# Performance work log

Hardware: AMD Instinct MI355X
Metric: run time of the kernel (lower is better)

## Reference

```python
import jax, jax.numpy as jnp
import numpy as np

N = 60000    # total nodes
E = 600000   # total edges
R = 7        # num relations (edge types)
D_IN = 64    # raw node feature dim
D = 128      # hidden_channels
D2 = 64      # hidden_channels // 2
L = 2        # num_layers
EPS = 1e-5   # LayerNorm eps (torch default)


def setup_inputs() -> dict:
    key = jax.random.key(0)
    ks = jax.random.split(key, 10)
    s = 0.05  # xavier-ish scale
    return {
        "x": jax.random.normal(ks[0], (N, D_IN), jnp.float32),
        "edge_index": jax.random.randint(ks[1], (2, E), 0, N, dtype=jnp.int64),
        "edge_type": jax.random.randint(ks[2], (E,), 0, R, dtype=jnp.int64),
        "emb_W": jax.random.normal(ks[3], (D_IN, D), jnp.float32) * s,
        "emb_b": jnp.zeros((D,), jnp.float32),
        "rel_W": jax.random.normal(ks[4], (L, R, D, D), jnp.float32) * s,
        "root_W": jax.random.normal(ks[5], (L, D, D), jnp.float32) * s,
        "conv_b": jnp.zeros((L, D), jnp.float32),
        "ln_g": jnp.ones((L, D), jnp.float32),
        "ln_b": jnp.zeros((L, D), jnp.float32),
        "cls_W1": jax.random.normal(ks[6], (D, D2), jnp.float32) * s,
        "cls_b1": jnp.zeros((D2,), jnp.float32),
        "cls_ln_g": jnp.ones((D2,), jnp.float32),
        "cls_ln_b": jnp.zeros((D2,), jnp.float32),
        "cls_W2": jax.random.normal(ks[7], (D2, 1), jnp.float32) * s,
        "cls_b2": jnp.zeros((1,), jnp.float32),
    }


def _layernorm(h, g, b):
    m = h.mean(-1, keepdims=True)
    v = h.var(-1, keepdims=True)  # population variance, matches torch LayerNorm
    return (h - m) * jax.lax.rsqrt(v + EPS) * g + b


def _rgcn_conv(h, Wrel, Wroot, b, src, dst, edge_type):
    # Transform every node by every relation weight: [R*N, D]
    t = jnp.einsum('nd,rde->rne', h, Wrel).reshape(R * N, D)
    msg = t[edge_type * N + src]                      # [E, D] per-edge messages
    seg = edge_type * N + dst                         # per-(relation, dst) segments
    summed = jax.ops.segment_sum(msg, seg, num_segments=R * N)
    cnt = jax.ops.segment_sum(jnp.ones((E,), msg.dtype), seg, num_segments=R * N)
    mean = summed / jnp.maximum(cnt, 1.0)[:, None]    # scatter-mean per relation
    agg = mean.reshape(R, N, D).sum(0)                # sum over relations
    return agg + h @ Wroot + b


def reference(x, edge_index, edge_type, emb_W, emb_b, rel_W, root_W, conv_b,
              ln_g, ln_b, cls_W1, cls_b1, cls_ln_g, cls_ln_b, cls_W2, cls_b2):
    src, dst = edge_index[0], edge_index[1]
    # Node embedding (features clamped as in original forward)
    h = jnp.clip(x, -10.0, 10.0) @ emb_W + emb_b
    for l in range(L):
        h = _rgcn_conv(h, rel_W[l], root_W[l], conv_b[l], src, dst, edge_type)
        h = jax.nn.relu(_layernorm(h, ln_g[l], ln_b[l]))
        # dropout is identity at inference
    # Classifier on transaction nodes (= all nodes in this unified setup)
    z = jax.nn.relu(_layernorm(h @ cls_W1 + cls_b1, cls_ln_g, cls_ln_b))
    return z @ cls_W2 + cls_b2  # [N, 1] logits
```

## Files before the change

### kernel.cpp

```cpp
#include <hip/hip_runtime.h>
#include <hip/hip_bf16.h>

typedef unsigned int uint;
typedef unsigned short ushort;

#define N_NODES 60000
#define N_EDGES 600000
#define NREL 7
#define D_IN 64
#define DHID 128
#define LEPS 1e-5f
#define EMB_BLKS 938
#define ROW_BLKS 469
#define SCAT_BLKS 512

typedef __attribute__((ext_vector_type(8))) short bf16x8v;
typedef __attribute__((ext_vector_type(4))) float f32x4v;

#define AS1C(p) ((const __attribute__((address_space(1))) void*)(p))
#define AS3(p)  ((__attribute__((address_space(3))) void*)(p))

__device__ __forceinline__ float bf2f(uint u16) {
    return __uint_as_float(u16 << 16);
}
__device__ __forceinline__ uint f2bf(float f) {
    uint u = __float_as_uint(f);
    uint lsb = (u >> 16) & 1u;
    u += 0x7fffu + lsb;
    return u >> 16;
}
__device__ __forceinline__ uint pack2(float a, float b) {
    return f2bf(a) | (f2bf(b) << 16);
}

__global__ __launch_bounds__(256) void k_prep(const float* __restrict__ relW,
                                              const float* __restrict__ rootW,
                                              const float* __restrict__ embW,
                                              const int* __restrict__ dst,
                                              const int* __restrict__ et,
                                              ushort* __restrict__ Btr,
                                              ushort* __restrict__ Bte,
                                              int* __restrict__ deg8) {
    __shared__ float t[64][65];
    const int tid = threadIdx.x;
    if (blockIdx.x < 64) {
        const int l  = blockIdx.x >> 5;
        const int b5 = blockIdx.x & 31;
        const int r  = b5 >> 2;
        const int kt = (b5 >> 1) & 1;
        const int jt = b5 & 1;
        #pragma unroll
        for (int i = 0; i < 4; ++i) {
            const int idx = i * 256 + tid;
            const int kr = idx >> 4;
            const int j4 = idx & 15;
            const int kg = kt * 64 + kr;
            const float* src = (r < 7)
                ? (relW + (((size_t)l * 7 + r) * 128 + kg) * 128 + jt * 64 + j4 * 4)
                : (rootW + ((size_t)l * 128 + kg) * 128 + jt * 64 + j4 * 4);
            const float4 v = *(const float4*)src;
            t[kr][j4 * 4 + 0] = v.x; t[kr][j4 * 4 + 1] = v.y;
            t[kr][j4 * 4 + 2] = v.z; t[kr][j4 * 4 + 3] = v.w;
        }
        __syncthreads();
        uint* btd = (uint*)Btr;
        #pragma unroll
        for (int i = 0; i < 8; ++i) {
            const int idx = i * 256 + tid;
            const int jr = idx >> 5;
            const int kd = idx & 31;
            const uint w = pack2(t[kd * 2][jr], t[kd * 2 + 1][jr]);
            btd[((size_t)(l * 8 + r) * 128 + jt * 64 + jr) * 64 + kt * 32 + kd] = w;
        }
    } else if (blockIdx.x < 66) {
        const int jt = blockIdx.x - 64;
        #pragma unroll
        for (int i = 0; i < 4; ++i) {
            const int idx = i * 256 + tid;
            const int kr = idx >> 4;
            const int j4 = idx & 15;
            const float4 v = *(const float4*)(embW + (size_t)kr * 128 + jt * 64 + j4 * 4);
            t[kr][j4 * 4 + 0] = v.x; t[kr][j4 * 4 + 1] = v.y;
            t[kr][j4 * 4 + 2] = v.z; t[kr][j4 * 4 + 3] = v.w;
        }
        __syncthreads();
        uint* btd = (uint*)Bte;
        #pragma unroll
        for (int i = 0; i < 8; ++i) {
            const int idx = i * 256 + tid;
            const int jr = idx >> 5;
            const int kd = idx & 31;
            const uint w = pack2(t[kd * 2][jr], t[kd * 2 + 1][jr]);
            btd[(size_t)(jt * 64 + jr) * 32 + kd] = w;
        }
    } else {
        for (int e = (blockIdx.x - 66) * 256 + tid; e < N_EDGES; e += 1024 * 256)
            atomicAdd(&deg8[dst[e] * 8 + et[e]], 1);
    }
}

__global__ void k_scan1n(const int* __restrict__ deg8, int* __restrict__ rp,
                         int* __restrict__ bsum, int n) {
    __shared__ int s[256];
    const int t = threadIdx.x;
    const int i = blockIdx.x * 256 + t;
    int v = 0;
    if (i < n) {
        const int4 x = *(const int4*)(deg8 + (size_t)i * 8);
        const int4 y = *(const int4*)(deg8 + (size_t)i * 8 + 4);
        v = x.x + x.y + x.z + x.w + y.x + y.y + y.z + y.w;
    }
    s[t] = v;
    __syncthreads();
    for (int o = 1; o < 256; o <<= 1) {
        int uu = (t >= o) ? s[t - o] : 0;
        __syncthreads();
        s[t] += uu;
        __syncthreads();
    }
    if (i < n) rp[i] = s[t] - v;
    if (t == 255) bsum[blockIdx.x] = s[255];
}
__global__ void k_scanmid(int* __restrict__ bs, int nb) {
    __shared__ int s[256];
    __shared__ int carrys;
    const int t = threadIdx.x;
    if (t == 0) carrys = 0;
    __syncthreads();
    const int nch = (nb + 255) / 256;
    for (int ch = 0; ch < nch; ++ch) {
        const int i = ch * 256 + t;
        const int v = (i < nb) ? bs[i] : 0;
        s[t] = v;
        __syncthreads();
        for (int o = 1; o < 256; o <<= 1) {
            int uu = (t >= o) ? s[t - o] : 0;
            __syncthreads();
            s[t] += uu;
            __syncthreads();
        }
        const int carry = carrys;
        if (i < nb) bs[i] = s[t] - v + carry;
        __syncthreads();
        if (t == 255) carrys = carry + s[255];
        __syncthreads();
    }
}
__global__ void k_scanadd(int* __restrict__ a, const int* __restrict__ bsums,
                          int* __restrict__ fill, int n) {
    const int i = blockIdx.x * 256 + threadIdx.x;
    if (i < n) {
        const int v = a[i] + bsums[blockIdx.x];
        a[i] = v;
        fill[i] = v;
    }
    if (blockIdx.x == 0 && threadIdx.x == 0) a[n] = N_EDGES;
}

__global__ __launch_bounds__(256) void k_emb(const float* __restrict__ x,
                                             const ushort* __restrict__ Bte,
                                             const float* __restrict__ ebias,
                                             ushort* __restrict__ h) {
    __shared__ alignas(16) ushort sa[64 * 64];
    __shared__ alignas(16) ushort sb[128 * 64];
    const int tid = threadIdx.x;
    const int lane = tid & 63;
    const int wid = tid >> 6;
    const int wrow = wid >> 1, wcol = wid & 1;
    const int l15 = lane & 15, lh = lane >> 4;
    const int row0 = blockIdx.x * 64;

    #pragma unroll
    for (int i = 0; i < 2; ++i) {
        const int p = i * 256 + tid;
        const int row = p >> 3, gq = p & 7;
        const int n = min(row0 + row, N_NODES - 1);
        const float4 xa = *(const float4*)(x + (size_t)n * 64 + gq * 8);
        const float4 xb = *(const float4*)(x + (size_t)n * 64 + gq * 8 + 4);
        uint w[4];
        w[0] = pack2(fminf(fmaxf(xa.x, -10.f), 10.f), fminf(fmaxf(xa.y, -10.f), 10.f));
        w[1] = pack2(fminf(fmaxf(xa.z, -10.f), 10.f), fminf(fmaxf(xa.w, -10.f), 10.f));
        w[2] = pack2(fminf(fmaxf(xb.x, -10.f), 10.f), fminf(fmaxf(xb.y, -10.f), 10.f));
        w[3] = pack2(fminf(fmaxf(xb.z, -10.f), 10.f), fminf(fmaxf(xb.w, -10.f), 10.f));
        *(uint4*)&sa[(row * 8 + (gq ^ (row & 7))) * 8] = make_uint4(w[0], w[1], w[2], w[3]);
    }
    #pragma unroll
    for (int i = 0; i < 4; ++i) {
        const int p = i * 256 + tid;
        const int row = p >> 3, gq = p & 7;
        const uint4 v = *(const uint4*)((const uint*)Bte + (size_t)row * 32 + gq * 4);
        *(uint4*)&sb[(row * 8 + (gq ^ (row & 7))) * 8] = v;
    }
    float bv[4];
    #pragma unroll
    for (int fn = 0; fn < 4; ++fn) bv[fn] = ebias[wcol * 64 + fn * 16 + l15];
    __syncthreads();

    f32x4v acc[2][4];
    #pragma unroll
    for (int fm = 0; fm < 2; ++fm)
        #pragma unroll
        for (int fn = 0; fn < 4; ++fn)
            acc[fm][fn] = (f32x4v){0.f, 0.f, 0.f, 0.f};
    #pragma unroll
    for (int kh = 0; kh < 2; ++kh) {
        bf16x8v af[2], bfr[4];
        #pragma unroll
        for (int fm = 0; fm < 2; ++fm) {
            const int rowa = wrow * 32 + fm * 16 + l15;
            const int slot = (kh * 4 + lh) ^ (rowa & 7);
            af[fm] = *(const bf16x8v*)&sa[rowa * 64 + slot * 8];
        }
        #pragma unroll
        for (int fn = 0; fn < 4; ++fn) {
            const int rowb = wcol * 64 + fn * 16 + l15;
            const int slot = (kh * 4 + lh) ^ (rowb & 7);
            bfr[fn] = *(const bf16x8v*)&sb[rowb * 64 + slot * 8];
        }
        #pragma unroll
        for (int fm = 0; fm < 2; ++fm)
            #pragma unroll
            for (int fn = 0; fn < 4; ++fn)
                acc[fm][fn] = __builtin_amdgcn_mfma_f32_16x16x32_bf16(
                    af[fm], bfr[fn], acc[fm][fn], 0, 0, 0);
    }
    #pragma unroll
    for (int fm = 0; fm < 2; ++fm)
        #pragma unroll
        for (int r = 0; r < 4; ++r) {
            const int row = row0 + wrow * 32 + fm * 16 + lh * 4 + r;
            if (row < N_NODES) {
                #pragma unroll
                for (int fn = 0; fn < 4; ++fn) {
                    const int col = wcol * 64 + fn * 16 + l15;
                    h[(size_t)row * 128 + col] = (ushort)f2bf(acc[fm][fn][r] + bv[fn]);
                }
            }
        }
}

__global__ __launch_bounds__(512) void k_transcat(const ushort* __restrict__ h16,
                                                  const ushort* __restrict__ Btr,
                                                  ushort* __restrict__ T16,
                                                  const int* __restrict__ src,
                                                  const int* __restrict__ dst,
                                                  const int* __restrict__ et,
                                                  int* __restrict__ fill,
                                                  uint* __restrict__ csr32,
                                                  int nscat) {
    __shared__ alignas(16) ushort sa[2][8192];
    __shared__ alignas(16) ushort sb[2][8192];
    const int tid = threadIdx.x;
    if (blockIdx.x < nscat) {
        for (int e = blockIdx.x * 512 + tid; e < N_EDGES; e += SCAT_BLKS * 512) {
            const int d = dst[e];
            const int r = et[e];
            const int p = atomicAdd(&fill[d], 1);
            csr32[p] = ((uint)r << 20) | (uint)(r * N_NODES + src[e]);
        }
        return;
    }
    const int lin = blockIdx.x - nscat;
    const int bj = lin & 7;
    const int row0 = (lin >> 3) * 128;
    const int lane = tid & 63;
    const int wid = tid >> 6;
    const int wrow = wid >> 1, wcol = wid & 1;
    const int l15 = lane & 15, lh = lane >> 4;

    int prow[2], pG[2], arow[2];
    #pragma unroll
    for (int hf = 0; hf < 2; ++hf) {
        const int p = hf * 512 + wid * 64 + lane;
        const int r = p >> 3;
        prow[hf] = r;
        pG[hf] = (p & 7) ^ (r & 7);
        arow[hf] = min(row0 + r, N_NODES - 1);
    }
    #pragma unroll
    for (int kt = 0; kt < 2; ++kt) {
        #pragma unroll
        for (int hf = 0; hf < 2; ++hf) {
            const ushort* ga = h16 + (size_t)arow[hf] * 128 + kt * 64 + pG[hf] * 8;
            __builtin_amdgcn_global_load_lds(AS1C(ga),
                AS3(&sa[kt][(hf * 512 + wid * 64) * 8]), 16, 0, 0);
            const ushort* gb = Btr + ((size_t)bj * 128 + prow[hf]) * 128 + kt * 64 + pG[hf] * 8;
            __builtin_amdgcn_global_load_lds(AS1C(gb),
                AS3(&sb[kt][(hf * 512 + wid * 64) * 8]), 16, 0, 0);
        }
    }
    __syncthreads();

    f32x4v acc[2][4];
    #pragma unroll
    for (int fm = 0; fm < 2; ++fm)
        #pragma unroll
        for (int fn = 0; fn < 4; ++fn)
            acc[fm][fn] = (f32x4v){0.f, 0.f, 0.f, 0.f};

    #pragma unroll
    for (int kt = 0; kt < 2; ++kt)
        #pragma unroll
        for (int kh = 0; kh < 2; ++kh) {
            bf16x8v af[2], bfr[4];
            #pragma unroll
            for (int fm = 0; fm < 2; ++fm) {
                const int rowa = wrow * 32 + fm * 16 + l15;
                const int slot = (kh * 4 + lh) ^ (rowa & 7);
                af[fm] = *(const bf16x8v*)&sa[kt][rowa * 64 + slot * 8];
            }
            #pragma unroll
            for (int fn = 0; fn < 4; ++fn) {
                const int rowb = wcol * 64 + fn * 16 + l15;
                const int slot = (kh * 4 + lh) ^ (rowb & 7);
                bfr[fn] = *(const bf16x8v*)&sb[kt][rowb * 64 + slot * 8];
            }
            #pragma unroll
            for (int fm = 0; fm < 2; ++fm)
                #pragma unroll
                for (int fn = 0; fn < 4; ++fn)
                    acc[fm][fn] = __builtin_amdgcn_mfma_f32_16x16x32_bf16(
                        af[fm], bfr[fn], acc[fm][fn], 0, 0, 0);
        }

    #pragma unroll
    for (int fm = 0; fm < 2; ++fm)
        #pragma unroll
        for (int r = 0; r < 4; ++r) {
            const int row = row0 + wrow * 32 + fm * 16 + lh * 4 + r;
            if (row < N_NODES) {
                ushort* tp = T16 + ((size_t)bj * N_NODES + row) * 128 + wcol * 64 + l15;
                #pragma unroll
                for (int fn = 0; fn < 4; ++fn)
                    tp[fn * 16] = (ushort)f2bf(acc[fm][fn][r]);
            }
        }
}

__global__ __launch_bounds__(256) void k_gather(const uint* __restrict__ T32,
                                                const int* __restrict__ rp,
                                                const int* __restrict__ deg8,
                                                const uint* __restrict__ csr32,
                                                const float* __restrict__ bias,
                                                const float* __restrict__ g,
                                                const float* __restrict__ bb,
                                                uint* __restrict__ hout) {
    __shared__ float sinv[4][8];
    const int wave = (blockIdx.x * 256 + threadIdx.x) >> 6;
    const int lane = threadIdx.x & 63;
    const int wid = (threadIdx.x >> 6) & 3;
    const int nwaves = gridDim.x * 4;
    const float2 bias2 = *(const float2*)(bias + 2 * lane);
    const float2 g2 = *(const float2*)(g + 2 * lane);
    const float2 b2 = *(const float2*)(bb + 2 * lane);
    #pragma unroll 1
    for (int n0 = wave; n0 < N_NODES; n0 += nwaves) {
        const int n = __builtin_amdgcn_readfirstlane(n0);
        const int beg = __builtin_amdgcn_readfirstlane(rp[n]);
        const int end = __builtin_amdgcn_readfirstlane(rp[n + 1]);
        if (lane < 8) {
            const int c = deg8[(size_t)n * 8 + lane];
            sinv[wid][lane] = 1.0f / (float)max(c, 1);
        }
        float ax = 0.f, ay = 0.f;
        #pragma unroll 1
        for (int e = beg; e < end; e += 8) {
            const int4 c0 = *(const int4*)(csr32 + e);
            const int4 c1 = *(const int4*)(csr32 + e + 4);
            int t[8] = {c0.x, c0.y, c0.z, c0.w, c1.x, c1.y, c1.z, c1.w};
            #pragma unroll
            for (int q = 0; q < 8; ++q) t[q] = __builtin_amdgcn_readfirstlane(t[q]);
            uint v[8];
            #pragma unroll
            for (int q = 0; q < 8; ++q)
                if (e + q < end) v[q] = T32[(size_t)(t[q] & 0xFFFFF) * 64 + lane];
            #pragma unroll
            for (int q = 0; q < 8; ++q)
                if (e + q < end) {
                    const float w = sinv[wid][(t[q] >> 20) & 7];
                    ax += w * __uint_as_float(v[q] << 16);
                    ay += w * __uint_as_float(v[q] & 0xFFFF0000u);
                }
        }
        const uint vr = T32[((size_t)7 * N_NODES + n) * 64 + lane];
        const float c0f = ax + bf2f(vr & 0xFFFFu) + bias2.x;
        const float c1f = ay + bf2f(vr >> 16) + bias2.y;
        float s = c0f + c1f, sq = c0f * c0f + c1f * c1f;
        #pragma unroll
        for (int o = 1; o < 64; o <<= 1) {
            s += __shfl_xor(s, o, 64);
            sq += __shfl_xor(sq, o, 64);
        }
        const float mean = s * (1.f / 128.f);
        const float var = sq * (1.f / 128.f) - mean * mean;
        const float rs = rsqrtf(var + LEPS);
        const float y0 = fmaxf((c0f - mean) * rs * g2.x + b2.x, 0.f);
        const float y1 = fmaxf((c1f - mean) * rs * g2.y + b2.y, 0.f);
        hout[(size_t)n * 64 + lane] = pack2(y0, y1);
    }
}

__global__ __launch_bounds__(256) void k_cls(const ushort* __restrict__ h16,
                                             const float* __restrict__ W1,
                                             const float* __restrict__ b1,
                                             const float* __restrict__ lg,
                                             const float* __restrict__ lb,
                                             const float* __restrict__ W2,
                                             const float* __restrict__ b2,
                                             float* __restrict__ outp, int nrows) {
    __shared__ ushort Bs[16 * 64 * 8];
    const int tid = threadIdx.x;
    #pragma unroll
    for (int i = 0; i < 8; ++i) {
        const int q = i * 256 + tid;
        const int k = q >> 4;
        const int j0 = (q & 15) * 4;
        const float4 w = *(const float4*)(W1 + (size_t)k * 64 + j0);
        const int gg = k >> 3, kp = k & 7;
        const int jx = (gg & 3) << 4;
        Bs[(gg * 64 + ((j0 + 0) ^ jx)) * 8 + kp] = (ushort)f2bf(w.x);
        Bs[(gg * 64 + ((j0 + 1) ^ jx)) * 8 + kp] = (ushort)f2bf(w.y);
        Bs[(gg * 64 + ((j0 + 2) ^ jx)) * 8 + kp] = (ushort)f2bf(w.z);
        Bs[(gg * 64 + ((j0 + 3) ^ jx)) * 8 + kp] = (ushort)f2bf(w.w);
    }
    const int lane = tid & 63, wid = tid >> 6;
    const int l15 = lane & 15, lh = lane >> 4;
    float lgv[4], lbv[4], w2v[4], b1v[4];
    #pragma unroll
    for (int fn = 0; fn < 4; ++fn) {
        const int col = fn * 16 + l15;
        lgv[fn] = lg[col]; lbv[fn] = lb[col]; w2v[fn] = W2[col]; b1v[fn] = b1[col];
    }
    const float b2v = b2[0];
    __syncthreads();

    const int row0 = blockIdx.x * 128;
    f32x4v acc[2][4];
    #pragma unroll
    for (int fm = 0; fm < 2; ++fm)
        #pragma unroll
        for (int fn = 0; fn < 4; ++fn)
            acc[fm][fn] = (f32x4v){0.f, 0.f, 0.f, 0.f};

    #pragma unroll
    for (int kk = 0; kk < 4; ++kk) {
        bf16x8v af[2], bfr[4];
        #pragma unroll
        for (int fm = 0; fm < 2; ++fm) {
            const int row = min(row0 + wid * 32 + fm * 16 + l15, nrows - 1);
            af[fm] = *(const bf16x8v*)(h16 + (size_t)row * 128 + kk * 32 + lh * 8);
        }
        #pragma unroll
        for (int fn = 0; fn < 4; ++fn) {
            const int gg = kk * 4 + lh;
            const int jc = fn * 16 + l15;
            bfr[fn] = *(const bf16x8v*)&Bs[(gg * 64 + (jc ^ ((gg & 3) << 4))) * 8];
        }
        #pragma unroll
        for (int fm = 0; fm < 2; ++fm)
            #pragma unroll
            for (int fn = 0; fn < 4; ++fn)
                acc[fm][fn] = __builtin_amdgcn_mfma_f32_16x16x32_bf16(
                    af[fm], bfr[fn], acc[fm][fn], 0, 0, 0);
    }

    #pragma unroll
    for (int fm = 0; fm < 2; ++fm)
        #pragma unroll
        for (int r = 0; r < 4; ++r) {
            float cv[4];
            float s = 0.f, sq = 0.f;
            #pragma unroll
            for (int fn = 0; fn < 4; ++fn) {
                cv[fn] = acc[fm][fn][r] + b1v[fn];
                s += cv[fn]; sq += cv[fn] * cv[fn];
            }
            s += __shfl_xor(s, 1, 64); sq += __shfl_xor(sq, 1, 64);
            s += __shfl_xor(s, 2, 64); sq += __shfl_xor(sq, 2, 64);
            s += __shfl_xor(s, 4, 64); sq += __shfl_xor(sq, 4, 64);
            s += __shfl_xor(s, 8, 64); sq += __shfl_xor(sq, 8, 64);
            const float mean = s * (1.f / 64.f);
            const float var = sq * (1.f / 64.f) - mean * mean;
            const float rs = rsqrtf(var + LEPS);
            float dot = 0.f;
            #pragma unroll
            for (int fn = 0; fn < 4; ++fn)
                dot += fmaxf((cv[fn] - mean) * rs * lgv[fn] + lbv[fn], 0.f) * w2v[fn];
            dot += __shfl_xor(dot, 1, 64);
            dot += __shfl_xor(dot, 2, 64);
            dot += __shfl_xor(dot, 4, 64);
            dot += __shfl_xor(dot, 8, 64);
            const int row = row0 + wid * 32 + fm * 16 + lh * 4 + r;
            if (l15 == 0 && row < nrows) outp[row] = dot + b2v;
        }
}

extern "C" void kernel_launch(void* const* d_in, const int* in_sizes, int n_in,
                              void* d_out, int out_size, void* d_ws, size_t ws_size,
                              hipStream_t stream) {
    const float* x      = (const float*)d_in[0];
    const int*   eidx   = (const int*)d_in[1];
    const int*   etype  = (const int*)d_in[2];
    const float* emb_W  = (const float*)d_in[3];
    const float* emb_b  = (const float*)d_in[4];
    const float* rel_W  = (const float*)d_in[5];
    const float* root_W = (const float*)d_in[6];
    const float* conv_b = (const float*)d_in[7];
    const float* ln_g   = (const float*)d_in[8];
    const float* ln_b   = (const float*)d_in[9];
    const float* cls_W1 = (const float*)d_in[10];
    const float* cls_b1 = (const float*)d_in[11];
    const float* cls_lg = (const float*)d_in[12];
    const float* cls_lb = (const float*)d_in[13];
    const float* cls_W2 = (const float*)d_in[14];
    const float* cls_b2 = (const float*)d_in[15];

    const int* srcv = eidx;
    const int* dstv = eidx + N_EDGES;

    char* ws = (char*)d_ws;
    size_t off = 0;
    auto alloc = [&](size_t bytes) { void* p = ws + off; off += (bytes + 255) & ~(size_t)255; return p; };
    ushort* h     = (ushort*)alloc((size_t)N_NODES * 128 * 2);
    ushort* T     = (ushort*)alloc((size_t)8 * N_NODES * 128 * 2);
    int*    rp    = (int*)alloc((size_t)(N_NODES + 1) * 4);
    int*    cnts  = (int*)alloc((size_t)(N_NODES * 9) * 4);
    uint*   csr32 = (uint*)alloc((size_t)(N_EDGES + 8) * 4);
    ushort* Btr   = (ushort*)alloc((size_t)2 * 8 * 128 * 128 * 2);
    ushort* Bte   = (ushort*)alloc((size_t)128 * 64 * 2);
    int*    bs    = (int*)alloc(4096);
    int*    deg8  = cnts;
    int*    fill  = cnts + N_NODES * 8;
    (void)ws_size; (void)n_in; (void)in_sizes; (void)out_size;

    const int SB = (N_NODES + 255) / 256;

    hipMemsetAsync(deg8, 0, (size_t)(N_NODES * 8) * 4, stream);
    k_prep<<<66 + 1024, 256, 0, stream>>>(rel_W, root_W, emb_W, dstv, etype,
                                          Btr, Bte, deg8);
    k_scan1n<<<SB, 256, 0, stream>>>(deg8, rp, bs, N_NODES);
    k_scanmid<<<1, 256, 0, stream>>>(bs, SB);
    k_scanadd<<<SB, 256, 0, stream>>>(rp, bs, fill, N_NODES);
    k_emb<<<EMB_BLKS, 256, 0, stream>>>(x, Bte, emb_b, h);

    k_transcat<<<SCAT_BLKS + 8 * ROW_BLKS, 512, 0, stream>>>(
        h, Btr, T, srcv, dstv, etype, fill, csr32, SCAT_BLKS);
    k_gather<<<2048, 256, 0, stream>>>(
        (const uint*)T, rp, deg8, csr32,
        conv_b, ln_g, ln_b, (uint*)h);

    k_transcat<<<8 * ROW_BLKS, 512, 0, stream>>>(
        h, Btr + (size_t)131072, T, srcv, dstv, etype, fill, csr32, 0);
    k_gather<<<2048, 256, 0, stream>>>(
        (const uint*)T, rp, deg8, csr32,
        conv_b + 128, ln_g + 128, ln_b + 128, (uint*)h);

    k_cls<<<469, 256, 0, stream>>>(h, cls_W1, cls_b1, cls_lg, cls_lb,
                                   cls_W2, cls_b2, (float*)d_out, N_NODES);
}
```

Measured before the change: 226.8 us.

## Loop all eight relation weights per block, reusing A tile with double-buffered B

Each transform block now loads its 128-row tile of h once into LDS and loops over all eight weight matrices (seven relations plus root), prefetching the next weight tile into a second LDS buffer while computing the current one. This removes the redundant reloading of the same h tile by eight separate blocks and overlaps the weight loads with MFMA work. In exchange the grid shrinks from about 3750 to 469 compute blocks, each with more LDS (96KB) and serial work, which lowers occupancy and parallelism across CUs. Leftover unused variables (prow, pG, arow) remain.

Result: faster. 218.1 us (-3.8%).

```diff
diff --git a/kernel.cpp b/kernel.cpp
--- a/kernel.cpp
+++ b/kernel.cpp
@@ -239,17 +239,17 @@
         }
 }
 
-__global__ __launch_bounds__(512) void k_transcat(const ushort* __restrict__ h16,
-                                                  const ushort* __restrict__ Btr,
-                                                  ushort* __restrict__ T16,
-                                                  const int* __restrict__ src,
-                                                  const int* __restrict__ dst,
-                                                  const int* __restrict__ et,
-                                                  int* __restrict__ fill,
-                                                  uint* __restrict__ csr32,
-                                                  int nscat) {
+__global__ __launch_bounds__(512) void k_trans8(const ushort* __restrict__ h16,
+                                                const ushort* __restrict__ Btr,
+                                                ushort* __restrict__ T16,
+                                                const int* __restrict__ src,
+                                                const int* __restrict__ dst,
+                                                const int* __restrict__ et,
+                                                int* __restrict__ fill,
+                                                uint* __restrict__ csr32,
+                                                int nscat) {
     __shared__ alignas(16) ushort sa[2][8192];
-    __shared__ alignas(16) ushort sb[2][8192];
+    __shared__ alignas(16) ushort sb[2][2][8192];
     const int tid = threadIdx.x;
     if (blockIdx.x < nscat) {
         for (int e = blockIdx.x * 512 + tid; e < N_EDGES; e += SCAT_BLKS * 512) {
@@ -260,81 +260,102 @@
         }
         return;
     }
-    const int lin = blockIdx.x - nscat;
-    const int bj = lin & 7;
-    const int row0 = (lin >> 3) * 128;
+    const int row0 = (blockIdx.x - nscat) * 128;
     const int lane = tid & 63;
     const int wid = tid >> 6;
     const int wrow = wid >> 1, wcol = wid & 1;
     const int l15 = lane & 15, lh = lane >> 4;
 
-    int prow[2], pG[2], arow[2];
+    int prow, pG, arow;
+    {
+        const int p = wid * 64 + lane;
+    }
+    int rA[2], gA[2], aw[2];
     #pragma unroll
     for (int hf = 0; hf < 2; ++hf) {
-        const int p = hf * 512 + wid * 64 + lane;
+        const int p = hf * 512 + tid;
         const int r = p >> 3;
-        prow[hf] = r;
-        pG[hf] = (p & 7) ^ (r & 7);
-        arow[hf] = min(row0 + r, N_NODES - 1);
-    }
-    #pragma unroll
-    for (int kt = 0; kt < 2; ++kt) {
-        #pragma unroll
-        for (int hf = 0; hf < 2; ++hf) {
-            const ushort* ga = h16 + (size_t)arow[hf] * 128 + kt * 64 + pG[hf] * 8;
-            __builtin_amdgcn_global_load_lds(AS1C(ga),
-                AS3(&sa[kt][(hf * 512 + wid * 64) * 8]), 16, 0, 0);
-            const ushort* gb = Btr + ((size_t)bj * 128 + prow[hf]) * 128 + kt * 64 + pG[hf] * 8;
-            __builtin_amdgcn_global_load_lds(AS1C(gb),
-                AS3(&sb[kt][(hf * 512 + wid * 64) * 8]), 16, 0, 0);
-        }
-    }
-    __syncthreads();
-
-    f32x4v acc[2][4];
-    #pragma unroll
-    for (int fm = 0; fm < 2; ++fm)
-        #pragma unroll
-        for (int fn = 0; fn < 4; ++fn)
-            acc[fm][fn] = (f32x4v){0.f, 0.f, 0.f, 0.f};
-
-    #pragma unroll
-    for (int kt = 0; kt < 2; ++kt)
-        #pragma unroll
-        for (int kh = 0; kh < 2; ++kh) {
-            bf16x8v af[2], bfr[4];
-            #pragma unroll
-            for (int fm = 0; fm < 2; ++fm) {
-                const int rowa = wrow * 32 + fm * 16 + l15;
-                const int slot = (kh * 4 + lh) ^ (rowa & 7);
-                af[fm] = *(const bf16x8v*)&sa[kt][rowa * 64 + slot * 8];
+        rA[hf] = r;
+        gA[hf] = (p & 7) ^ (r & 7);
+        aw[hf] = min(row0 + r, N_NODES - 1);
+    }
+    auto stageA = [&]() {
+        #pragma unroll
+        for (int kt = 0; kt < 2; ++kt)
+            #pragma unroll
+            for (int hf = 0; hf < 2; ++hf) {
+                const ushort* ga = h16 + (size_t)aw[hf] * 128 + kt * 64 + gA[hf] * 8;
+                __builtin_amdgcn_global_load_lds(AS1C(ga),
+                    AS3(&sa[kt][(hf * 512 + tid) * 8]), 16, 0, 0);
             }
-            #pragma unroll
-            for (int fn = 0; fn < 4; ++fn) {
-                const int rowb = wcol * 64 + fn * 16 + l15;
-                const int slot = (kh * 4 + lh) ^ (rowb & 7);
-                bfr[fn] = *(const bf16x8v*)&sb[kt][rowb * 64 + slot * 8];
+    };
+    auto stageB = [&](int buf, int bj) {
+        #pragma unroll
+        for (int kt = 0; kt < 2; ++kt)
+            #pragma unroll
+            for (int hf = 0; hf < 2; ++hf) {
+                const ushort* gb = Btr + ((size_t)bj * 128 + rA[hf]) * 128 + kt * 64 + gA[hf] * 8;
+                __builtin_amdgcn_global_load_lds(AS1C(gb),
+                    AS3(&sb[buf][kt][(hf * 512 + tid) * 8]), 16, 0, 0);
             }
-            #pragma unroll
-            for (int fm = 0; fm < 2; ++fm)
+    };
+
+    stageA();
+    stageB(0, 0);
+
+    #pragma unroll 1
+    for (int bj = 0; bj < 8; ++bj) {
+        const int cur = bj & 1;
+        if (bj < 7) {
+            stageB(cur ^ 1, bj + 1);
+            asm volatile("s_waitcnt vmcnt(4)\n\ts_barrier" ::: "memory");
+        } else {
+            asm volatile("s_waitcnt vmcnt(0)\n\ts_barrier" ::: "memory");
+        }
+        f32x4v acc[2][4];
+        #pragma unroll
+        for (int fm = 0; fm < 2; ++fm)
+            #pragma unroll
+            for (int fn = 0; fn < 4; ++fn)
+                acc[fm][fn] = (f32x4v){0.f, 0.f, 0.f, 0.f};
+        #pragma unroll
+        for (int kt = 0; kt < 2; ++kt)
+            #pragma unroll
+            for (int kh = 0; kh < 2; ++kh) {
+                bf16x8v af[2], bfr[4];
                 #pragma unroll
-                for (int fn = 0; fn < 4; ++fn)
-                    acc[fm][fn] = __builtin_amdgcn_mfma_f32_16x16x32_bf16(
-                        af[fm], bfr[fn], acc[fm][fn], 0, 0, 0);
-        }
-
-    #pragma unroll
-    for (int fm = 0; fm < 2; ++fm)
-        #pragma unroll
-        for (int r = 0; r < 4; ++r) {
-            const int row = row0 + wrow * 32 + fm * 16 + lh * 4 + r;
-            if (row < N_NODES) {
-                ushort* tp = T16 + ((size_t)bj * N_NODES + row) * 128 + wcol * 64 + l15;
+                for (int fm = 0; fm < 2; ++fm) {
+                    const int rowa = wrow * 32 + fm * 16 + l15;
+                    const int slot = (kh * 4 + lh) ^ (rowa & 7);
+                    af[fm] = *(const bf16x8v*)&sa[kt][rowa * 64 + slot * 8];
+                }
                 #pragma unroll
-                for (int fn = 0; fn < 4; ++fn)
-                    tp[fn * 16] = (ushort)f2bf(acc[fm][fn][r]);
+                for (int fn = 0; fn < 4; ++fn) {
+                    const int rowb = wcol * 64 + fn * 16 + l15;
+                    const int slot = (kh * 4 + lh) ^ (rowb & 7);
+                    bfr[fn] = *(const bf16x8v*)&sb[cur][kt][rowb * 64 + slot * 8];
+                }
+                #pragma unroll
+                for (int fm = 0; fm < 2; ++fm)
+                    #pragma unroll
+                    for (int fn = 0; fn < 4; ++fn)
+                        acc[fm][fn] = __builtin_amdgcn_mfma_f32_16x16x32_bf16(
+                            af[fm], bfr[fn], acc[fm][fn], 0, 0, 0);
             }
-        }
+        #pragma unroll
+        for (int fm = 0; fm < 2; ++fm)
+            #pragma unroll
+            for (int r = 0; r < 4; ++r) {
+                const int row = row0 + wrow * 32 + fm * 16 + lh * 4 + r;
+                if (row < N_NODES) {
+                    ushort* tp = T16 + ((size_t)bj * N_NODES + row) * 128 + wcol * 64 + l15;
+                    #pragma unroll
+                    for (int fn = 0; fn < 4; ++fn)
+                        tp[fn * 16] = (ushort)f2bf(acc[fm][fn][r]);
+                }
+            }
+        asm volatile("s_barrier" ::: "memory");
+    }
 }
 
 __global__ __launch_bounds__(256) void k_gather(const uint* __restrict__ T32,
@@ -543,13 +564,13 @@
     k_scanadd<<<SB, 256, 0, stream>>>(rp, bs, fill, N_NODES);
     k_emb<<<EMB_BLKS, 256, 0, stream>>>(x, Bte, emb_b, h);
 
-    k_transcat<<<SCAT_BLKS + 8 * ROW_BLKS, 512, 0, stream>>>(
+    k_trans8<<<SCAT_BLKS + ROW_BLKS, 512, 0, stream>>>(
         h, Btr, T, srcv, dstv, etype, fill, csr32, SCAT_BLKS);
     k_gather<<<2048, 256, 0, stream>>>(
         (const uint*)T, rp, deg8, csr32,
         conv_b, ln_g, ln_b, (uint*)h);
 
-    k_transcat<<<8 * ROW_BLKS, 512, 0, stream>>>(
+    k_trans8<<<ROW_BLKS, 512, 0, stream>>>(
         h, Btr + (size_t)131072, T, srcv, dstv, etype, fill, csr32, 0);
     k_gather<<<2048, 256, 0, stream>>>(
         (const uint*)T, rp, deg8, csr32,
```
